# Kernel tuning notes

Measured on AMD Instinct MI355X. Metric: run time of the kernel, lower is better.

Reference implementation:

```python
import jax, jax.numpy as jnp
import numpy as np

N = 50000        # nodes
E = 1600000      # edges (avg degree 32)
DIM_IN = 128
H = 4            # num_heads
D1 = 100         # gc1 per-head out dim
D2 = 20          # gc2 per-head out dim
B = 64           # graphs in the batch
EPS = 1e-5
SLOPE = 0.01     # torch leaky_relu default


def setup_inputs() -> dict:
    key = jax.random.key(0)
    ks = jax.random.split(key, 16)
    sc = lambda fan: 1.0 / np.sqrt(fan)
    inp = {
        'feat': jax.random.normal(ks[0], (N, DIM_IN), jnp.float32),
        'src': jax.random.randint(ks[1], (E,), 0, N, jnp.int32),
        'dst': jax.random.randint(ks[2], (E,), 0, N, jnp.int32),
        'graph_id': jnp.sort(jax.random.randint(ks[3], (N,), 0, B, jnp.int32)),
        # GAT layer 1: per-head fc weight [H, din, dout], attn vector [H, 2*dout]
        'W1': jax.random.normal(ks[4], (H, DIM_IN, D1), jnp.float32) * sc(DIM_IN),
        'a1': jax.random.normal(ks[5], (H, 2 * D1), jnp.float32) * sc(2 * D1),
        # GAT layer 2 (input is cat of heads: H*D1 = 400)
        'W2': jax.random.normal(ks[6], (H, H * D1, D2), jnp.float32) * sc(H * D1),
        'a2': jax.random.normal(ks[7], (H, 2 * D2), jnp.float32) * sc(2 * D2),
        # readout MLP 20 -> 128 -> 32 -> 1
        'Wf1': jax.random.normal(ks[8], (D2, 128), jnp.float32) * sc(D2),
        'bf1': jnp.zeros((128,), jnp.float32),
        'Wf2': jax.random.normal(ks[9], (128, 32), jnp.float32) * sc(128),
        'bf2': jnp.zeros((32,), jnp.float32),
        'Wf3': jax.random.normal(ks[10], (32, 1), jnp.float32) * sc(32),
        'bf3': jnp.zeros((1,), jnp.float32),
        'gamma2': jnp.ones((32,), jnp.float32),   # bn2 weight
        'beta2': jnp.zeros((32,), jnp.float32),   # bn2 bias
    }
    return inp


def _gat_heads(h, W, a, src, dst):
    """Per-head GAT: gather-attn -> segment softmax over dst mailboxes -> scatter-sum.
    Returns list of [N, dout] head outputs. Loop over H=4 heads (small fixed set)."""
    outs = []
    for i in range(W.shape[0]):
        z = h @ W[i]                               # [N, dout]
        d = z.shape[1]
        s_src = z @ a[i, :d]                       # [N] (attn split: a.[z_src,z_dst])
        s_dst = z @ a[i, d:]                       # [N]
        e = jax.nn.leaky_relu(s_src[src] + s_dst[dst], SLOPE)   # [E]
        m = jax.ops.segment_max(e, dst, num_segments=N)          # stable softmax max
        ex = jnp.exp(e - m[dst])
        den = jax.ops.segment_sum(ex, dst, num_segments=N)
        alpha = ex / den[dst]                      # [E] segment softmax
        outs.append(jax.ops.segment_sum(alpha[:, None] * z[src], dst, num_segments=N))
    return outs


def reference(feat, src, dst, graph_id, W1, a1, W2, a2,
              Wf1, bf1, Wf2, bf2, Wf3, bf3, gamma2, beta2):
    src = src.astype(jnp.int32); dst = dst.astype(jnp.int32)
    h = jax.nn.relu(jnp.concatenate(_gat_heads(feat, W1, a1, src, dst), axis=1))  # [N,400]
    h = jax.nn.relu(jnp.mean(jnp.stack(_gat_heads(h, W2, a2, src, dst), 0), 0))   # [N,20]
    # dgl.mean_nodes: per-graph mean of node features
    counts = jax.ops.segment_sum(jnp.ones((N,), h.dtype), graph_id, num_segments=B)
    hg = jax.ops.segment_sum(h, graph_id, num_segments=B) / counts[:, None]        # [B,20]
    out = jax.nn.relu(hg @ Wf1 + bf1)              # dropout = identity (eval)
    out = out @ Wf2 + bf2                          # [B,32]
    mu = jnp.mean(out, axis=0)                     # BatchNorm1d (training stats, biased var)
    var = jnp.mean((out - mu) ** 2, axis=0)
    out = jax.nn.relu(gamma2 * (out - mu) * jax.lax.rsqrt(var + EPS) + beta2)
    return out @ Wf3 + bf3                         # [B,1]
```

## Files before the change

kernel.cpp:

```cpp
#include <hip/hip_runtime.h>
#include <hip/hip_bf16.h>
#include <math.h>

#define N_NODES 50000
#define N_EDGES 1600000
#define DIN 128
#define NH 4
#define D1 100
#define D2 20
#define NB 64
#define EPS_BN 1e-5f


typedef unsigned int uint;
typedef unsigned short ushort;
typedef short short8v __attribute__((ext_vector_type(8)));
typedef float float4v __attribute__((ext_vector_type(4)));

__device__ __forceinline__ void bf16x2_unpack(uint p, float& lo, float& hi) {
  lo = __uint_as_float(p << 16);
  hi = __uint_as_float(p & 0xffff0000u);
}

__device__ __forceinline__ ushort f2bf(float f) {
  uint u = __float_as_uint(f);
  return (ushort)((u + 0x7fffu + ((u >> 16) & 1u)) >> 16);
}

__global__ void prep_b1t(const float* __restrict__ W1, ushort* __restrict__ B1t) {
  int o = blockIdx.x * 256 + threadIdx.x;
  int h = o >> 14;
  int r = o & 16383;
  int j = r >> 7, k = r & 127;
  float v = (j < D1) ? W1[((size_t)h * DIN + k) * D1 + j] : 0.f;
  B1t[o] = f2bf(v);
}

__global__ void prep_b2t(const float* __restrict__ W2, ushort* __restrict__ B2t) {
  int idx = blockIdx.x * 256 + threadIdx.x;
  if (idx >= 80 * 416) return;
  int c = idx / 416, k = idx - c * 416;
  int h = c / D2, j = c - h * D2;
  float v = (k < NH * D1) ? W2[((size_t)h * (NH * D1) + k) * D2 + j] : 0.f;
  B2t[idx] = f2bf(v);
}

__global__ __launch_bounds__(256) void gemm1_mfma(const float* __restrict__ feat,
                                                  const ushort* __restrict__ B1t,
                                                  ushort* __restrict__ z1b) {
  __shared__ __align__(16) short As[64 * 136];
  __shared__ __align__(16) short Bs[128 * 136];
  const int row0 = blockIdx.x * 64;
  const int h = blockIdx.y;
  const int tid = threadIdx.x;
#pragma unroll
  for (int it = 0; it < 8; it++) {
    int idx = tid + it * 256;
    int r = idx >> 5, c4 = idx & 31;
    int row = row0 + r;
    float4 v = make_float4(0.f, 0.f, 0.f, 0.f);
    if (row < N_NODES) v = *reinterpret_cast<const float4*>(feat + (size_t)row * DIN + c4 * 4);
    short4 s;
    s.x = (short)f2bf(v.x); s.y = (short)f2bf(v.y);
    s.z = (short)f2bf(v.z); s.w = (short)f2bf(v.w);
    *reinterpret_cast<short4*>(&As[r * 136 + c4 * 4]) = s;
  }
  {
    const uint* bsrc = reinterpret_cast<const uint*>(B1t + (size_t)h * 16384);
#pragma unroll
    for (int it = 0; it < 32; it++) {
      int idx = tid + it * 256;
      int j = idx >> 6, kk = idx & 63;
      *reinterpret_cast<uint*>(&Bs[j * 136 + kk * 2]) = bsrc[idx];
    }
  }
  __syncthreads();
  const int wv = tid >> 6, lane = tid & 63;
  const int m = lane & 15, q = lane >> 4;
  float4v acc[8];
#pragma unroll
  for (int t = 0; t < 8; t++) acc[t] = (float4v){0.f, 0.f, 0.f, 0.f};
#pragma unroll
  for (int kq = 0; kq < 4; kq++) {
    short8v a = *reinterpret_cast<const short8v*>(&As[(wv * 16 + m) * 136 + kq * 32 + q * 8]);
#pragma unroll
    for (int t = 0; t < 8; t++) {
      short8v b = *reinterpret_cast<const short8v*>(&Bs[(t * 16 + m) * 136 + kq * 32 + q * 8]);
      acc[t] = __builtin_amdgcn_mfma_f32_16x16x32_bf16(a, b, acc[t], 0, 0, 0);
    }
  }
#pragma unroll
  for (int t = 0; t < 8; t++) {
    int cl = t * 16 + m;
    if (cl < D1) {
#pragma unroll
      for (int reg = 0; reg < 4; reg++) {
        int row = row0 + wv * 16 + q * 4 + reg;
        if (row < N_NODES) z1b[(size_t)row * (NH * D1) + h * D1 + cl] = f2bf(acc[t][reg]);
      }
    }
  }
}

__global__ __launch_bounds__(256) void gemm2_mfma(const ushort* __restrict__ h1b,
                                                  const ushort* __restrict__ B2t,
                                                  ushort* __restrict__ z2b) {
  __shared__ __align__(16) short As[64 * 40];
  __shared__ __align__(16) short Bs[80 * 40];
  const int row0 = blockIdx.x * 64;
  const int tid = threadIdx.x;
  const int wv = tid >> 6, lane = tid & 63;
  const int m = lane & 15, q = lane >> 4;
  const uint* au = reinterpret_cast<const uint*>(h1b);
  const uint* bu = reinterpret_cast<const uint*>(B2t);
  uint* asu = reinterpret_cast<uint*>(As);
  uint* bsu = reinterpret_cast<uint*>(Bs);
  float4v acc[5];
#pragma unroll
  for (int t = 0; t < 5; t++) acc[t] = (float4v){0.f, 0.f, 0.f, 0.f};
  for (int ch = 0; ch < 13; ch++) {
    int k0u = ch * 16;
    {
      int idx = tid;
#pragma unroll
      for (int it = 0; it < 4; it++, idx += 256) {
        int r = idx >> 4, ku = idx & 15;
        int row = row0 + r;
        uint v = 0;
        if (row < N_NODES && (k0u + ku) < 200) v = au[(size_t)row * 200 + k0u + ku];
        asu[r * 20 + ku] = v;
      }
      idx = tid;
#pragma unroll
      for (int it = 0; it < 5; it++, idx += 256) {
        int c = idx >> 4, ku = idx & 15;
        bsu[c * 20 + ku] = bu[(size_t)c * 208 + k0u + ku];
      }
    }
    __syncthreads();
    short8v a = *reinterpret_cast<const short8v*>(&As[(wv * 16 + m) * 40 + q * 8]);
#pragma unroll
    for (int t = 0; t < 5; t++) {
      short8v b = *reinterpret_cast<const short8v*>(&Bs[(t * 16 + m) * 40 + q * 8]);
      acc[t] = __builtin_amdgcn_mfma_f32_16x16x32_bf16(a, b, acc[t], 0, 0, 0);
    }
    __syncthreads();
  }
#pragma unroll
  for (int t = 0; t < 5; t++) {
    int col = t * 16 + m;
#pragma unroll
    for (int reg = 0; reg < 4; reg++) {
      int row = row0 + wv * 16 + q * 4 + reg;
      if (row < N_NODES) z2b[(size_t)row * (NH * D2) + col] = f2bf(acc[t][reg]);
    }
  }
}

template <int DOUT>
__global__ void scores_kernel(const ushort* __restrict__ z,
                              const float* __restrict__ a,
                              float* __restrict__ ssrc,
                              float* __restrict__ sdst) {
  int t = blockIdx.x * blockDim.x + threadIdx.x;
  if (t >= N_NODES * NH) return;
  int n = t >> 2;
  int h = t & 3;
  const uint* zr = reinterpret_cast<const uint*>(z) + (size_t)n * (NH * DOUT / 2) + h * (DOUT / 2);
  const float* as = a + h * 2 * DOUT;
  const float* ad = as + DOUT;
  float s1 = 0.f, s2 = 0.f;
  for (int j = 0; j < DOUT / 2; j++) {
    float lo, hi;
    bf16x2_unpack(zr[j], lo, hi);
    s1 += lo * as[2 * j] + hi * as[2 * j + 1];
    s2 += lo * ad[2 * j] + hi * ad[2 * j + 1];
  }
  ssrc[h * N_NODES + n] = s1;
  sdst[h * N_NODES + n] = s2;
}

__global__ void hist_kernel(const int* __restrict__ dst, int* __restrict__ cnt) {
  int e = blockIdx.x * blockDim.x + threadIdx.x;
  if (e < N_EDGES) atomicAdd(&cnt[dst[e]], 1);
}

__global__ __launch_bounds__(512) void scan1_kernel(const int* __restrict__ cnt,
                                                    int* __restrict__ row_ptr,
                                                    int* __restrict__ btot, int n) {
  __shared__ int ws[8];
  int b = blockIdx.x, tid = threadIdx.x, lane = tid & 63, wv = tid >> 6;
  int i = b * 512 + tid;
  int v = (i < n) ? cnt[i] : 0;
  int orig = v;
  for (int off = 1; off < 64; off <<= 1) {
    int t = __shfl_up(v, off);
    if (lane >= off) v += t;
  }
  if (lane == 63) ws[wv] = v;
  __syncthreads();
  int wo = 0;
  for (int j = 0; j < wv; j++) wo += ws[j];
  if (i < n) row_ptr[i] = wo + v - orig;
  if (tid == 511) btot[b] = wo + v;
}

__global__ __launch_bounds__(128) void scan2_kernel(int* __restrict__ btot,
                                                    int* __restrict__ row_ptr_n, int nb) {
  __shared__ int ws2[2];
  int tid = threadIdx.x, lane = tid & 63, wv = tid >> 6;
  int v = (tid < nb) ? btot[tid] : 0;
  int orig = v;
  for (int off = 1; off < 64; off <<= 1) {
    int t = __shfl_up(v, off);
    if (lane >= off) v += t;
  }
  if (lane == 63) ws2[wv] = v;
  __syncthreads();
  int wo = (wv == 1) ? ws2[0] : 0;
  if (tid < nb) btot[tid] = wo + v - orig;
  if (tid == nb - 1) *row_ptr_n = wo + v;
}

__global__ __launch_bounds__(512) void scan3_kernel(int* __restrict__ row_ptr,
                                                    int* __restrict__ cursor,
                                                    const int* __restrict__ btot, int n) {
  int i = blockIdx.x * 512 + threadIdx.x;
  if (i < n) {
    int v = row_ptr[i] + btot[blockIdx.x];
    row_ptr[i] = v;
    cursor[i] = v;
  }
}

__global__ void fill_kernel(const int* __restrict__ src, const int* __restrict__ dst,
                            int* __restrict__ cursor, int* __restrict__ csr_src) {
  int e = blockIdx.x * blockDim.x + threadIdx.x;
  if (e < N_EDGES) {
    int p = atomicAdd(&cursor[dst[e]], 1);
    csr_src[p] = src[e];
  }
}

__global__ __launch_bounds__(256) void agg1_kernel(const ushort* __restrict__ z,
                                                   const float* __restrict__ ssrc,
                                                   const float* __restrict__ sdst,
                                                   const int* __restrict__ row_ptr,
                                                   const int* __restrict__ csr_src,
                                                   ushort* __restrict__ h1b) {
  __shared__ float lw[NH][128];
  const int d = blockIdx.x;
  const int h = threadIdx.x >> 6, lane = threadIdx.x & 63;
  const int beg = row_ptr[d], end = row_ptr[d + 1];
  const int deg = end - beg;
  uint* h1u = reinterpret_cast<uint*>(h1b);
  const size_t ou = (size_t)d * 200 + h * 50 + lane;
  const bool act = lane < D1 / 2;
  if (deg == 0) {
    if (act) h1u[ou] = 0u;
    return;
  }
  const int hN = h * N_NODES;
  const float sd = sdst[hN + d];
  const uint* zb = reinterpret_cast<const uint*>(z);
  const int hco = h * 50 + lane;
  float den = 0.f;
  float aE0 = 0.f, aE1 = 0.f, aE2 = 0.f, aE3 = 0.f;
  float aO0 = 0.f, aO1 = 0.f, aO2 = 0.f, aO3 = 0.f;
  for (int c0 = 0; c0 < deg; c0 += 128) {
    const int cn = min(128, deg - c0);
    const int cb = beg + c0;
    for (int i = lane; i < cn; i += 64) {
      int s = csr_src[cb + i];
      float e = ssrc[hN + s] + sd;
      e = fmaxf(e, 0.01f * e);
      float x = __expf(e);
      lw[h][i] = x;
      den += x;
    }
    if (act) {
      int j = 0;
      for (; j + 8 <= cn; j += 8) {
        int s0 = csr_src[cb + j + 0], s1 = csr_src[cb + j + 1];
        int s2 = csr_src[cb + j + 2], s3 = csr_src[cb + j + 3];
        int s4 = csr_src[cb + j + 4], s5 = csr_src[cb + j + 5];
        int s6 = csr_src[cb + j + 6], s7 = csr_src[cb + j + 7];
        float x0 = lw[h][j + 0], x1 = lw[h][j + 1];
        float x2 = lw[h][j + 2], x3 = lw[h][j + 3];
        float x4 = lw[h][j + 4], x5 = lw[h][j + 5];
        float x6 = lw[h][j + 6], x7 = lw[h][j + 7];
        uint p0 = zb[(size_t)s0 * 200 + hco];
        uint p1 = zb[(size_t)s1 * 200 + hco];
        uint p2 = zb[(size_t)s2 * 200 + hco];
        uint p3 = zb[(size_t)s3 * 200 + hco];
        uint p4 = zb[(size_t)s4 * 200 + hco];
        uint p5 = zb[(size_t)s5 * 200 + hco];
        uint p6 = zb[(size_t)s6 * 200 + hco];
        uint p7 = zb[(size_t)s7 * 200 + hco];
        float lo, hi;
        bf16x2_unpack(p0, lo, hi); aE0 += x0 * lo; aO0 += x0 * hi;
        bf16x2_unpack(p1, lo, hi); aE1 += x1 * lo; aO1 += x1 * hi;
        bf16x2_unpack(p2, lo, hi); aE2 += x2 * lo; aO2 += x2 * hi;
        bf16x2_unpack(p3, lo, hi); aE3 += x3 * lo; aO3 += x3 * hi;
        bf16x2_unpack(p4, lo, hi); aE0 += x4 * lo; aO0 += x4 * hi;
        bf16x2_unpack(p5, lo, hi); aE1 += x5 * lo; aO1 += x5 * hi;
        bf16x2_unpack(p6, lo, hi); aE2 += x6 * lo; aO2 += x6 * hi;
        bf16x2_unpack(p7, lo, hi); aE3 += x7 * lo; aO3 += x7 * hi;
      }
      for (; j < cn; j++) {
        int s = csr_src[cb + j];
        float x = lw[h][j];
        uint p = zb[(size_t)s * 200 + hco];
        float lo, hi;
        bf16x2_unpack(p, lo, hi);
        aE0 += x * lo;
        aO0 += x * hi;
      }
    }
  }
#pragma unroll
  for (int off = 32; off > 0; off >>= 1) den += __shfl_xor(den, off);
  if (!act) return;
  float inv = 1.0f / den;
  float vE = ((aE0 + aE1) + (aE2 + aE3)) * inv;
  float vO = ((aO0 + aO1) + (aO2 + aO3)) * inv;
  vE = vE > 0.f ? vE : 0.f;
  vO = vO > 0.f ? vO : 0.f;
  h1u[ou] = (uint)f2bf(vE) | ((uint)f2bf(vO) << 16);
}

__global__ __launch_bounds__(256) void agg2_kernel(const ushort* __restrict__ z,
                                                   const float* __restrict__ ssrc,
                                                   const float* __restrict__ sdst,
                                                   const int* __restrict__ row_ptr,
                                                   const int* __restrict__ csr_src,
                                                   float* __restrict__ h2) {
  __shared__ float lw[NH][128];
  __shared__ float hbuf[NH][D2];
  const int d = blockIdx.x;
  const int h = threadIdx.x >> 6, lane = threadIdx.x & 63;
  const int beg = row_ptr[d], end = row_ptr[d + 1];
  const int deg = end - beg;
  const int g = lane / 10;
  const int j = lane - g * 10;
  if (deg > 0) {
    const int hN = h * N_NODES;
    const float sd = sdst[hN + d];
    const uint* zb = reinterpret_cast<const uint*>(z);
    const int hco = h * 10 + j;
    float den = 0.f, aE = 0.f, aO = 0.f;
    for (int c0 = 0; c0 < deg; c0 += 128) {
      const int cn = min(128, deg - c0);
      const int cb = beg + c0;
      for (int i = lane; i < cn; i += 64) {
        int s = csr_src[cb + i];
        float e = ssrc[hN + s] + sd;
        e = fmaxf(e, 0.01f * e);
        float x = __expf(e);
        lw[h][i] = x;
        den += x;
      }
      if (g < 6) {
        int i = g;
        for (; i + 6 < cn; i += 12) {
          int s0 = csr_src[cb + i];
          int s1 = csr_src[cb + i + 6];
          float x0 = lw[h][i];
          float x1 = lw[h][i + 6];
          uint p0 = zb[(size_t)s0 * 40 + hco];
          uint p1 = zb[(size_t)s1 * 40 + hco];
          float lo, hi;
          bf16x2_unpack(p0, lo, hi); aE += x0 * lo; aO += x0 * hi;
          bf16x2_unpack(p1, lo, hi); aE += x1 * lo; aO += x1 * hi;
        }
        if (i < cn) {
          int s = csr_src[cb + i];
          float x = lw[h][i];
          uint p = zb[(size_t)s * 40 + hco];
          float lo, hi;
          bf16x2_unpack(p, lo, hi);
          aE += x * lo;
          aO += x * hi;
        }
      }
    }
#pragma unroll
    for (int off = 32; off > 0; off >>= 1) den += __shfl_xor(den, off);
    float tE = aE, tO = aO;
#pragma unroll
    for (int k = 1; k < 6; k++) {
      tE += __shfl(aE, lane + 10 * k);
      tO += __shfl(aO, lane + 10 * k);
    }
    if (lane < 10) {
      float invd = 1.0f / den;
      hbuf[h][2 * j] = tE * invd;
      hbuf[h][2 * j + 1] = tO * invd;
    }
  } else {
    if (lane < 10) {
      hbuf[h][2 * j] = 0.f;
      hbuf[h][2 * j + 1] = 0.f;
    }
  }
  __syncthreads();
  if (threadIdx.x < D2) {
    int c = threadIdx.x;
    float m = 0.25f * (hbuf[0][c] + hbuf[1][c] + hbuf[2][c] + hbuf[3][c]);
    h2[(size_t)d * D2 + c] = m > 0.f ? m : 0.f;
  }
}

__global__ __launch_bounds__(256) void pool_kernel(const float* __restrict__ h2,
                                                   const int* __restrict__ gid,
                                                   float* __restrict__ hg,
                                                   int* __restrict__ gcnt) {
  int wave = threadIdx.x >> 6, lane = threadIdx.x & 63;
  int n = (blockIdx.x * 4 + wave) * 64 + lane;
  bool valid = n < N_NODES;
  int g = gid[valid ? n : (N_NODES - 1)];
  int g0 = __shfl(g, 0), g63 = __shfl(g, 63);
  unsigned long long mask = __ballot(valid);
  if (g0 == g63) {
    if (lane == 0) atomicAdd(&gcnt[g0], (int)__popcll(mask));
#pragma unroll
    for (int c = 0; c < D2; c++) {
      float v = valid ? h2[(size_t)n * D2 + c] : 0.f;
#pragma unroll
      for (int off = 32; off > 0; off >>= 1) v += __shfl_xor(v, off);
      if (lane == 0) atomicAdd(&hg[g0 * D2 + c], v);
    }
  } else if (valid) {
    atomicAdd(&gcnt[g], 1);
    for (int c = 0; c < D2; c++) atomicAdd(&hg[g * D2 + c], h2[(size_t)n * D2 + c]);
  }
}

__global__ __launch_bounds__(256) void head_kernel(const float* __restrict__ hg,
                                                   const int* __restrict__ gcnt,
                                                   const float* __restrict__ Wf1,
                                                   const float* __restrict__ bf1,
                                                   const float* __restrict__ Wf2,
                                                   const float* __restrict__ bf2,
                                                   const float* __restrict__ Wf3,
                                                   const float* __restrict__ bf3,
                                                   const float* __restrict__ gamma,
                                                   const float* __restrict__ beta,
                                                   float* __restrict__ out) {
  __shared__ float X[NB][D2];
  __shared__ float T1[NB][128];
  __shared__ float T2[NB][32];
  __shared__ float scale_s[32], shift_s[32];
  int tid = threadIdx.x;
  for (int i = tid; i < NB * D2; i += 256) {
    int r = i / D2, c = i % D2;
    X[r][c] = hg[i] / (float)gcnt[r];
  }
  __syncthreads();
  for (int i = tid; i < NB * 128; i += 256) {
    int r = i >> 7, c = i & 127;
    float s = bf1[c];
#pragma unroll
    for (int k = 0; k < D2; k++) s += X[r][k] * Wf1[k * 128 + c];
    T1[r][c] = s > 0.f ? s : 0.f;
  }
  __syncthreads();
  for (int i = tid; i < NB * 32; i += 256) {
    int r = i >> 5, c = i & 31;
    float s = bf2[c];
#pragma unroll
    for (int k = 0; k < 128; k++) s += T1[r][k] * Wf2[k * 32 + c];
    T2[r][c] = s;
  }
  __syncthreads();
  if (tid < 32) {
    float mu = 0.f;
    for (int r = 0; r < NB; r++) mu += T2[r][tid];
    mu *= (1.f / NB);
    float var = 0.f;
    for (int r = 0; r < NB; r++) {
      float dv = T2[r][tid] - mu;
      var += dv * dv;
    }
    var *= (1.f / NB);
    float sc = gamma[tid] * rsqrtf(var + EPS_BN);
    scale_s[tid] = sc;
    shift_s[tid] = beta[tid] - mu * sc;
  }
  __syncthreads();
  if (tid < NB) {
    float s = bf3[0];
#pragma unroll
    for (int c = 0; c < 32; c++) {
      float y = scale_s[c] * T2[tid][c] + shift_s[c];
      y = y > 0.f ? y : 0.f;
      s += y * Wf3[c];
    }
    out[tid] = s;
  }
}


extern "C" void kernel_launch(void* const* d_in, const int* in_sizes, int n_in,
                              void* d_out, int out_size, void* d_ws, size_t ws_size,
                              hipStream_t stream) {
  const float* feat = (const float*)d_in[0];
  const int* src = (const int*)d_in[1];
  const int* dst = (const int*)d_in[2];
  const int* gid = (const int*)d_in[3];
  const float* W1 = (const float*)d_in[4];
  const float* a1 = (const float*)d_in[5];
  const float* W2 = (const float*)d_in[6];
  const float* a2 = (const float*)d_in[7];
  const float* Wf1 = (const float*)d_in[8];
  const float* bf1 = (const float*)d_in[9];
  const float* Wf2 = (const float*)d_in[10];
  const float* bf2 = (const float*)d_in[11];
  const float* Wf3 = (const float*)d_in[12];
  const float* bf3 = (const float*)d_in[13];
  const float* gamma2 = (const float*)d_in[14];
  const float* beta2 = (const float*)d_in[15];
  float* outp = (float*)d_out;

  char* p = (char*)d_ws;
  auto alloc = [&](size_t bytes) {
    void* q = (void*)p;
    p += (bytes + 255) & ~(size_t)255;
    return q;
  };
  ushort* z1b = (ushort*)alloc((size_t)N_NODES * NH * D1 * 2);
  ushort* z2b = (ushort*)alloc((size_t)N_NODES * NH * D2 * 2);
  ushort* h1b = (ushort*)alloc((size_t)N_NODES * NH * D1 * 2);
  float* h2 = (float*)alloc((size_t)N_NODES * D2 * 4);
  float* ssrc = (float*)alloc((size_t)NH * N_NODES * 4);
  float* sdst = (float*)alloc((size_t)NH * N_NODES * 4);
  int* cnt = (int*)alloc((size_t)N_NODES * 4);
  int* row_ptr = (int*)alloc((size_t)(N_NODES + 1) * 4);
  int* cursor = (int*)alloc((size_t)N_NODES * 4);
  int* csr = (int*)alloc((size_t)N_EDGES * 4);
  int* btot = (int*)alloc((size_t)128 * 4);
  ushort* B1t = (ushort*)alloc((size_t)NH * 128 * 128 * 2);
  ushort* B2t = (ushort*)alloc((size_t)80 * 416 * 2);
  float* hg = (float*)alloc((size_t)NB * D2 * 4);
  int* gcnt = (int*)alloc((size_t)NB * 4);

  const int rows64 = (N_NODES + 63) / 64;
  const int eblk = (N_EDGES + 255) / 256;
  const int nblk = (N_NODES + 255) / 256;
  const int nhblk = (N_NODES * NH + 255) / 256;
  const int sblk = (N_NODES + 511) / 512;

  hipMemsetAsync(cnt, 0, (size_t)N_NODES * 4, stream);
  hist_kernel<<<eblk, 256, 0, stream>>>(dst, cnt);
  scan1_kernel<<<sblk, 512, 0, stream>>>(cnt, row_ptr, btot, N_NODES);
  scan2_kernel<<<1, 128, 0, stream>>>(btot, row_ptr + N_NODES, sblk);
  scan3_kernel<<<sblk, 512, 0, stream>>>(row_ptr, cursor, btot, N_NODES);
  fill_kernel<<<eblk, 256, 0, stream>>>(src, dst, cursor, csr);

  prep_b1t<<<256, 256, 0, stream>>>(W1, B1t);
  prep_b2t<<<130, 256, 0, stream>>>(W2, B2t);

  gemm1_mfma<<<dim3(rows64, NH), 256, 0, stream>>>(feat, B1t, z1b);
  scores_kernel<D1><<<nhblk, 256, 0, stream>>>(z1b, a1, ssrc, sdst);
  agg1_kernel<<<N_NODES, 256, 0, stream>>>(z1b, ssrc, sdst, row_ptr, csr, h1b);

  gemm2_mfma<<<rows64, 256, 0, stream>>>(h1b, B2t, z2b);
  scores_kernel<D2><<<nhblk, 256, 0, stream>>>(z2b, a2, ssrc, sdst);
  agg2_kernel<<<N_NODES, 256, 0, stream>>>(z2b, ssrc, sdst, row_ptr, csr, h2);

  hipMemsetAsync(hg, 0, (size_t)NB * D2 * 4, stream);
  hipMemsetAsync(gcnt, 0, (size_t)NB * 4, stream);
  pool_kernel<<<nblk, 256, 0, stream>>>(h2, gid, hg, gcnt);
  head_kernel<<<1, 256, 0, stream>>>(hg, gcnt, Wf1, bf1, Wf2, bf2, Wf3, bf3,
                                     gamma2, beta2, outp);
}
```

Baseline: 760.5 us.

## Pad z layouts per head and gather edges with 16-byte vector loads

The projected node features z1 and z2 are stored with per-head padding (104 and 24 bf16 elements per head), so each head slice is 16-byte aligned. The aggregation kernels then gather neighbour rows with uint4 loads. Lanes are split into groups that each handle different edges, and partial sums are combined with cross-lane shuffles. This cuts the number of gather instructions per edge and improves memory-transaction efficiency. In exchange it adds padding bytes, shuffle reductions, and partly idle lanes (for example, 13 of 16 lanes active per group in agg1).

Measured after the change: 797.8 us. 1.05x slower.

```diff
diff --git a/kernel.cpp b/kernel.cpp
--- a/kernel.cpp
+++ b/kernel.cpp
@@ -16,6 +16,12 @@
 typedef unsigned short ushort;
 typedef short short8v __attribute__((ext_vector_type(8)));
 typedef float float4v __attribute__((ext_vector_type(4)));
+typedef uint uint4v __attribute__((ext_vector_type(4)));
+
+#define Z1_ROWU 208
+#define Z1_HU 52
+#define Z2_ROWU 48
+#define Z2_HU 12
 
 __device__ __forceinline__ void bf16x2_unpack(uint p, float& lo, float& hi) {
   lo = __uint_as_float(p << 16);
@@ -92,11 +98,12 @@
 #pragma unroll
   for (int t = 0; t < 8; t++) {
     int cl = t * 16 + m;
-    if (cl < D1) {
+    if (cl < 104) {
 #pragma unroll
       for (int reg = 0; reg < 4; reg++) {
         int row = row0 + wv * 16 + q * 4 + reg;
-        if (row < N_NODES) z1b[(size_t)row * (NH * D1) + h * D1 + cl] = f2bf(acc[t][reg]);
+        if (row < N_NODES)
+          z1b[(size_t)row * 416 + h * 104 + cl] = (cl < D1) ? f2bf(acc[t][reg]) : (ushort)0;
       }
     }
   }
@@ -149,15 +156,17 @@
 #pragma unroll
   for (int t = 0; t < 5; t++) {
     int col = t * 16 + m;
+    int hh = col / 20;
+    int jj = col - hh * 20;
 #pragma unroll
     for (int reg = 0; reg < 4; reg++) {
       int row = row0 + wv * 16 + q * 4 + reg;
-      if (row < N_NODES) z2b[(size_t)row * (NH * D2) + col] = f2bf(acc[t][reg]);
-    }
-  }
-}
-
-template <int DOUT>
+      if (row < N_NODES) z2b[(size_t)row * 96 + hh * 24 + jj] = f2bf(acc[t][reg]);
+    }
+  }
+}
+
+template <int DOUT, int HEADU, int ROWU>
 __global__ void scores_kernel(const ushort* __restrict__ z,
                               const float* __restrict__ a,
                               float* __restrict__ ssrc,
@@ -166,7 +175,7 @@
   if (t >= N_NODES * NH) return;
   int n = t >> 2;
   int h = t & 3;
-  const uint* zr = reinterpret_cast<const uint*>(z) + (size_t)n * (NH * DOUT / 2) + h * (DOUT / 2);
+  const uint* zr = reinterpret_cast<const uint*>(z) + (size_t)n * ROWU + h * HEADU;
   const float* as = a + h * 2 * DOUT;
   const float* ad = as + DOUT;
   float s1 = 0.f, s2 = 0.f;
@@ -251,22 +260,28 @@
   __shared__ float lw[NH][128];
   const int d = blockIdx.x;
   const int h = threadIdx.x >> 6, lane = threadIdx.x & 63;
+  const int g = lane >> 4;
+  const int j = lane & 15;
   const int beg = row_ptr[d], end = row_ptr[d + 1];
   const int deg = end - beg;
   uint* h1u = reinterpret_cast<uint*>(h1b);
-  const size_t ou = (size_t)d * 200 + h * 50 + lane;
-  const bool act = lane < D1 / 2;
   if (deg == 0) {
-    if (act) h1u[ou] = 0u;
+    if (g == 0 && j < 13) {
+      int base = d * 200 + h * 50 + j * 4;
+      int nu = (j == 12) ? 2 : 4;
+      for (int u = 0; u < nu; u++) h1u[base + u] = 0u;
+    }
     return;
   }
   const int hN = h * N_NODES;
   const float sd = sdst[hN + d];
-  const uint* zb = reinterpret_cast<const uint*>(z);
-  const int hco = h * 50 + lane;
+  const uint* zu = reinterpret_cast<const uint*>(z);
+  const int zoff = h * Z1_HU + j * 4;
+  const bool act = (j < 13);
   float den = 0.f;
-  float aE0 = 0.f, aE1 = 0.f, aE2 = 0.f, aE3 = 0.f;
-  float aO0 = 0.f, aO1 = 0.f, aO2 = 0.f, aO3 = 0.f;
+  float acc[8];
+#pragma unroll
+  for (int t = 0; t < 8; t++) acc[t] = 0.f;
   for (int c0 = 0; c0 < deg; c0 += 128) {
     const int cn = min(128, deg - c0);
     const int cb = beg + c0;
@@ -279,54 +294,39 @@
       den += x;
     }
     if (act) {
-      int j = 0;
-      for (; j + 8 <= cn; j += 8) {
-        int s0 = csr_src[cb + j + 0], s1 = csr_src[cb + j + 1];
-        int s2 = csr_src[cb + j + 2], s3 = csr_src[cb + j + 3];
-        int s4 = csr_src[cb + j + 4], s5 = csr_src[cb + j + 5];
-        int s6 = csr_src[cb + j + 6], s7 = csr_src[cb + j + 7];
-        float x0 = lw[h][j + 0], x1 = lw[h][j + 1];
-        float x2 = lw[h][j + 2], x3 = lw[h][j + 3];
-        float x4 = lw[h][j + 4], x5 = lw[h][j + 5];
-        float x6 = lw[h][j + 6], x7 = lw[h][j + 7];
-        uint p0 = zb[(size_t)s0 * 200 + hco];
-        uint p1 = zb[(size_t)s1 * 200 + hco];
-        uint p2 = zb[(size_t)s2 * 200 + hco];
-        uint p3 = zb[(size_t)s3 * 200 + hco];
-        uint p4 = zb[(size_t)s4 * 200 + hco];
-        uint p5 = zb[(size_t)s5 * 200 + hco];
-        uint p6 = zb[(size_t)s6 * 200 + hco];
-        uint p7 = zb[(size_t)s7 * 200 + hco];
+      for (int i = g; i < cn; i += 4) {
+        int s = csr_src[cb + i];
+        float x = lw[h][i];
+        uint4v p = *reinterpret_cast<const uint4v*>(zu + (size_t)s * Z1_ROWU + zoff);
         float lo, hi;
-        bf16x2_unpack(p0, lo, hi); aE0 += x0 * lo; aO0 += x0 * hi;
-        bf16x2_unpack(p1, lo, hi); aE1 += x1 * lo; aO1 += x1 * hi;
-        bf16x2_unpack(p2, lo, hi); aE2 += x2 * lo; aO2 += x2 * hi;
-        bf16x2_unpack(p3, lo, hi); aE3 += x3 * lo; aO3 += x3 * hi;
-        bf16x2_unpack(p4, lo, hi); aE0 += x4 * lo; aO0 += x4 * hi;
-        bf16x2_unpack(p5, lo, hi); aE1 += x5 * lo; aO1 += x5 * hi;
-        bf16x2_unpack(p6, lo, hi); aE2 += x6 * lo; aO2 += x6 * hi;
-        bf16x2_unpack(p7, lo, hi); aE3 += x7 * lo; aO3 += x7 * hi;
-      }
-      for (; j < cn; j++) {
-        int s = csr_src[cb + j];
-        float x = lw[h][j];
-        uint p = zb[(size_t)s * 200 + hco];
-        float lo, hi;
-        bf16x2_unpack(p, lo, hi);
-        aE0 += x * lo;
-        aO0 += x * hi;
+        bf16x2_unpack(p.x, lo, hi); acc[0] += x * lo; acc[1] += x * hi;
+        bf16x2_unpack(p.y, lo, hi); acc[2] += x * lo; acc[3] += x * hi;
+        bf16x2_unpack(p.z, lo, hi); acc[4] += x * lo; acc[5] += x * hi;
+        bf16x2_unpack(p.w, lo, hi); acc[6] += x * lo; acc[7] += x * hi;
       }
     }
   }
 #pragma unroll
   for (int off = 32; off > 0; off >>= 1) den += __shfl_xor(den, off);
-  if (!act) return;
+#pragma unroll
+  for (int t = 0; t < 8; t++) {
+    acc[t] += __shfl_xor(acc[t], 32);
+    acc[t] += __shfl_xor(acc[t], 16);
+  }
+  if (g != 0 || j >= 13) return;
   float inv = 1.0f / den;
-  float vE = ((aE0 + aE1) + (aE2 + aE3)) * inv;
-  float vO = ((aO0 + aO1) + (aO2 + aO3)) * inv;
-  vE = vE > 0.f ? vE : 0.f;
-  vO = vO > 0.f ? vO : 0.f;
-  h1u[ou] = (uint)f2bf(vE) | ((uint)f2bf(vO) << 16);
+  int base = d * 200 + h * 50 + j * 4;
+  int nu = (j == 12) ? 2 : 4;
+#pragma unroll
+  for (int u = 0; u < 4; u++) {
+    if (u < nu) {
+      float vE = acc[2 * u] * inv;
+      float vO = acc[2 * u + 1] * inv;
+      vE = vE > 0.f ? vE : 0.f;
+      vO = vO > 0.f ? vO : 0.f;
+      h1u[base + u] = (uint)f2bf(vE) | ((uint)f2bf(vO) << 16);
+    }
+  }
 }
 
 __global__ __launch_bounds__(256) void agg2_kernel(const ushort* __restrict__ z,
@@ -339,16 +339,20 @@
   __shared__ float hbuf[NH][D2];
   const int d = blockIdx.x;
   const int h = threadIdx.x >> 6, lane = threadIdx.x & 63;
+  const int g = lane >> 2;
+  const int j = lane & 3;
   const int beg = row_ptr[d], end = row_ptr[d + 1];
   const int deg = end - beg;
-  const int g = lane / 10;
-  const int j = lane - g * 10;
   if (deg > 0) {
     const int hN = h * N_NODES;
     const float sd = sdst[hN + d];
-    const uint* zb = reinterpret_cast<const uint*>(z);
-    const int hco = h * 10 + j;
-    float den = 0.f, aE = 0.f, aO = 0.f;
+    const uint* zu = reinterpret_cast<const uint*>(z);
+    const int zoff = h * Z2_HU + j * 4;
+    const bool act = (j < 3);
+    float den = 0.f;
+    float acc[8];
+#pragma unroll
+    for (int t = 0; t < 8; t++) acc[t] = 0.f;
     for (int c0 = 0; c0 < deg; c0 += 128) {
       const int cn = min(128, deg - c0);
       const int cb = beg + c0;
@@ -360,47 +364,43 @@
         lw[h][i] = x;
         den += x;
       }
-      if (g < 6) {
-        int i = g;
-        for (; i + 6 < cn; i += 12) {
-          int s0 = csr_src[cb + i];
-          int s1 = csr_src[cb + i + 6];
-          float x0 = lw[h][i];
-          float x1 = lw[h][i + 6];
-          uint p0 = zb[(size_t)s0 * 40 + hco];
-          uint p1 = zb[(size_t)s1 * 40 + hco];
-          float lo, hi;
-          bf16x2_unpack(p0, lo, hi); aE += x0 * lo; aO += x0 * hi;
-          bf16x2_unpack(p1, lo, hi); aE += x1 * lo; aO += x1 * hi;
-        }
-        if (i < cn) {
+      if (act) {
+        for (int i = g; i < cn; i += 16) {
           int s = csr_src[cb + i];
           float x = lw[h][i];
-          uint p = zb[(size_t)s * 40 + hco];
+          uint4v p = *reinterpret_cast<const uint4v*>(zu + (size_t)s * Z2_ROWU + zoff);
           float lo, hi;
-          bf16x2_unpack(p, lo, hi);
-          aE += x * lo;
-          aO += x * hi;
+          bf16x2_unpack(p.x, lo, hi); acc[0] += x * lo; acc[1] += x * hi;
+          bf16x2_unpack(p.y, lo, hi); acc[2] += x * lo; acc[3] += x * hi;
+          bf16x2_unpack(p.z, lo, hi); acc[4] += x * lo; acc[5] += x * hi;
+          bf16x2_unpack(p.w, lo, hi); acc[6] += x * lo; acc[7] += x * hi;
         }
       }
     }
 #pragma unroll
     for (int off = 32; off > 0; off >>= 1) den += __shfl_xor(den, off);
-    float tE = aE, tO = aO;
-#pragma unroll
-    for (int k = 1; k < 6; k++) {
-      tE += __shfl(aE, lane + 10 * k);
-      tO += __shfl(aO, lane + 10 * k);
-    }
-    if (lane < 10) {
+#pragma unroll
+    for (int t = 0; t < 8; t++) {
+      acc[t] += __shfl_xor(acc[t], 4);
+      acc[t] += __shfl_xor(acc[t], 8);
+      acc[t] += __shfl_xor(acc[t], 16);
+      acc[t] += __shfl_xor(acc[t], 32);
+    }
+    if (lane < 3) {
       float invd = 1.0f / den;
-      hbuf[h][2 * j] = tE * invd;
-      hbuf[h][2 * j + 1] = tO * invd;
+#pragma unroll
+      for (int t = 0; t < 8; t++) {
+        int c = lane * 8 + t;
+        if (c < D2) hbuf[h][c] = acc[t] * invd;
+      }
     }
   } else {
-    if (lane < 10) {
-      hbuf[h][2 * j] = 0.f;
-      hbuf[h][2 * j + 1] = 0.f;
+    if (lane < 3) {
+#pragma unroll
+      for (int t = 0; t < 8; t++) {
+        int c = lane * 8 + t;
+        if (c < D2) hbuf[h][c] = 0.f;
+      }
     }
   }
   __syncthreads();
@@ -528,8 +528,8 @@
     p += (bytes + 255) & ~(size_t)255;
     return q;
   };
-  ushort* z1b = (ushort*)alloc((size_t)N_NODES * NH * D1 * 2);
-  ushort* z2b = (ushort*)alloc((size_t)N_NODES * NH * D2 * 2);
+  ushort* z1b = (ushort*)alloc((size_t)N_NODES * 416 * 2);
+  ushort* z2b = (ushort*)alloc((size_t)N_NODES * 96 * 2);
   ushort* h1b = (ushort*)alloc((size_t)N_NODES * NH * D1 * 2);
   float* h2 = (float*)alloc((size_t)N_NODES * D2 * 4);
   float* ssrc = (float*)alloc((size_t)NH * N_NODES * 4);
@@ -561,11 +561,11 @@
   prep_b2t<<<130, 256, 0, stream>>>(W2, B2t);
 
   gemm1_mfma<<<dim3(rows64, NH), 256, 0, stream>>>(feat, B1t, z1b);
-  scores_kernel<D1><<<nhblk, 256, 0, stream>>>(z1b, a1, ssrc, sdst);
+  scores_kernel<D1, Z1_HU, Z1_ROWU><<<nhblk, 256, 0, stream>>>(z1b, a1, ssrc, sdst);
   agg1_kernel<<<N_NODES, 256, 0, stream>>>(z1b, ssrc, sdst, row_ptr, csr, h1b);
 
   gemm2_mfma<<<rows64, 256, 0, stream>>>(h1b, B2t, z2b);
-  scores_kernel<D2><<<nhblk, 256, 0, stream>>>(z2b, a2, ssrc, sdst);
+  scores_kernel<D2, Z2_HU, Z2_ROWU><<<nhblk, 256, 0, stream>>>(z2b, a2, ssrc, sdst);
   agg2_kernel<<<N_NODES, 256, 0, stream>>>(z2b, ssrc, sdst, row_ptr, csr, h2);
 
   hipMemsetAsync(hg, 0, (size_t)NB * D2 * 4, stream);
```

## Pad z1/z2 rows to aligned strides and restructure agg2 to split edges across waves

Applied to the files above, without the earlier changes.

The z1 buffer is stored with a padded 448-element row (104 per head) and z2 with a 128-element row, so each gathered neighbour row begins on a larger aligned boundary and the agg kernels' row gathers touch fewer cache lines. agg2 is rewritten so each of the 4 waves handles a strided slice of 8-edge chunks covering all heads at once. It uses 40 lanes to gather an 80-element z2 row per edge, then reduces the partial sums and denominators across waves in shared memory. This raises parallelism per destination node and coalesces gathers, at the cost of more memory for the padded buffers and some idle lanes.

New measurement: 733.0 us. 1.04x faster.

```diff
diff --git a/kernel.cpp b/kernel.cpp
--- a/kernel.cpp
+++ b/kernel.cpp
@@ -16,6 +16,10 @@
 typedef unsigned short ushort;
 typedef short short8v __attribute__((ext_vector_type(8)));
 typedef float float4v __attribute__((ext_vector_type(4)));
+
+#define Z1_ROWU 224
+#define Z1_HU 52
+#define Z2_ROWU 64
 
 __device__ __forceinline__ void bf16x2_unpack(uint p, float& lo, float& hi) {
   lo = __uint_as_float(p << 16);
@@ -92,11 +96,12 @@
 #pragma unroll
   for (int t = 0; t < 8; t++) {
     int cl = t * 16 + m;
-    if (cl < D1) {
+    if (cl < 104) {
 #pragma unroll
       for (int reg = 0; reg < 4; reg++) {
         int row = row0 + wv * 16 + q * 4 + reg;
-        if (row < N_NODES) z1b[(size_t)row * (NH * D1) + h * D1 + cl] = f2bf(acc[t][reg]);
+        if (row < N_NODES)
+          z1b[(size_t)row * 448 + h * 104 + cl] = (cl < D1) ? f2bf(acc[t][reg]) : (ushort)0;
       }
     }
   }
@@ -152,12 +157,12 @@
 #pragma unroll
     for (int reg = 0; reg < 4; reg++) {
       int row = row0 + wv * 16 + q * 4 + reg;
-      if (row < N_NODES) z2b[(size_t)row * (NH * D2) + col] = f2bf(acc[t][reg]);
-    }
-  }
-}
-
-template <int DOUT>
+      if (row < N_NODES) z2b[(size_t)row * 128 + col] = f2bf(acc[t][reg]);
+    }
+  }
+}
+
+template <int DOUT, int HEADU, int ROWU>
 __global__ void scores_kernel(const ushort* __restrict__ z,
                               const float* __restrict__ a,
                               float* __restrict__ ssrc,
@@ -166,7 +171,7 @@
   if (t >= N_NODES * NH) return;
   int n = t >> 2;
   int h = t & 3;
-  const uint* zr = reinterpret_cast<const uint*>(z) + (size_t)n * (NH * DOUT / 2) + h * (DOUT / 2);
+  const uint* zr = reinterpret_cast<const uint*>(z) + (size_t)n * ROWU + h * HEADU;
   const float* as = a + h * 2 * DOUT;
   const float* ad = as + DOUT;
   float s1 = 0.f, s2 = 0.f;
@@ -263,7 +268,7 @@
   const int hN = h * N_NODES;
   const float sd = sdst[hN + d];
   const uint* zb = reinterpret_cast<const uint*>(z);
-  const int hco = h * 50 + lane;
+  const int hco = h * Z1_HU + lane;
   float den = 0.f;
   float aE0 = 0.f, aE1 = 0.f, aE2 = 0.f, aE3 = 0.f;
   float aO0 = 0.f, aO1 = 0.f, aO2 = 0.f, aO3 = 0.f;
@@ -289,14 +294,14 @@
         float x2 = lw[h][j + 2], x3 = lw[h][j + 3];
         float x4 = lw[h][j + 4], x5 = lw[h][j + 5];
         float x6 = lw[h][j + 6], x7 = lw[h][j + 7];
-        uint p0 = zb[(size_t)s0 * 200 + hco];
-        uint p1 = zb[(size_t)s1 * 200 + hco];
-        uint p2 = zb[(size_t)s2 * 200 + hco];
-        uint p3 = zb[(size_t)s3 * 200 + hco];
-        uint p4 = zb[(size_t)s4 * 200 + hco];
-        uint p5 = zb[(size_t)s5 * 200 + hco];
-        uint p6 = zb[(size_t)s6 * 200 + hco];
-        uint p7 = zb[(size_t)s7 * 200 + hco];
+        uint p0 = zb[(size_t)s0 * Z1_ROWU + hco];
+        uint p1 = zb[(size_t)s1 * Z1_ROWU + hco];
+        uint p2 = zb[(size_t)s2 * Z1_ROWU + hco];
+        uint p3 = zb[(size_t)s3 * Z1_ROWU + hco];
+        uint p4 = zb[(size_t)s4 * Z1_ROWU + hco];
+        uint p5 = zb[(size_t)s5 * Z1_ROWU + hco];
+        uint p6 = zb[(size_t)s6 * Z1_ROWU + hco];
+        uint p7 = zb[(size_t)s7 * Z1_ROWU + hco];
         float lo, hi;
         bf16x2_unpack(p0, lo, hi); aE0 += x0 * lo; aO0 += x0 * hi;
         bf16x2_unpack(p1, lo, hi); aE1 += x1 * lo; aO1 += x1 * hi;
@@ -310,7 +315,7 @@
       for (; j < cn; j++) {
         int s = csr_src[cb + j];
         float x = lw[h][j];
-        uint p = zb[(size_t)s * 200 + hco];
+        uint p = zb[(size_t)s * Z1_ROWU + hco];
         float lo, hi;
         bf16x2_unpack(p, lo, hi);
         aE0 += x * lo;
@@ -335,79 +340,77 @@
                                                    const int* __restrict__ row_ptr,
                                                    const int* __restrict__ csr_src,
                                                    float* __restrict__ h2) {
-  __shared__ float lw[NH][128];
-  __shared__ float hbuf[NH][D2];
+  __shared__ float xw[4][8][4];
+  __shared__ int sw[4][8];
+  __shared__ float accb[4][40][2];
+  __shared__ float denb[4][4];
   const int d = blockIdx.x;
-  const int h = threadIdx.x >> 6, lane = threadIdx.x & 63;
-  const int beg = row_ptr[d], end = row_ptr[d + 1];
-  const int deg = end - beg;
-  const int g = lane / 10;
-  const int j = lane - g * 10;
-  if (deg > 0) {
-    const int hN = h * N_NODES;
-    const float sd = sdst[hN + d];
-    const uint* zb = reinterpret_cast<const uint*>(z);
-    const int hco = h * 10 + j;
-    float den = 0.f, aE = 0.f, aO = 0.f;
-    for (int c0 = 0; c0 < deg; c0 += 128) {
-      const int cn = min(128, deg - c0);
-      const int cb = beg + c0;
-      for (int i = lane; i < cn; i += 64) {
-        int s = csr_src[cb + i];
-        float e = ssrc[hN + s] + sd;
-        e = fmaxf(e, 0.01f * e);
-        float x = __expf(e);
-        lw[h][i] = x;
-        den += x;
+  const int wv = threadIdx.x >> 6, lane = threadIdx.x & 63;
+  const int beg = row_ptr[d];
+  const int deg = row_ptr[d + 1] - beg;
+  if (deg == 0) {
+    if (threadIdx.x < D2) h2[(size_t)d * D2 + threadIdx.x] = 0.f;
+    return;
+  }
+  const int eh_h = lane & 3, eh_e = lane >> 2;
+  const int hq = lane / 10;
+  const uint* zu = reinterpret_cast<const uint*>(z);
+  float sd = 0.f;
+  if (lane < 32) sd = sdst[eh_h * N_NODES + d];
+  float den = 0.f;
+  float acc0 = 0.f, acc1 = 0.f;
+  for (int c0 = wv * 8; c0 < deg; c0 += 32) {
+    const int cn = min(8, deg - c0);
+    const int cb = beg + c0;
+    if (lane < 32) {
+      int ee = (eh_e < cn) ? eh_e : 0;
+      int s = csr_src[cb + ee];
+      float e = ssrc[eh_h * N_NODES + s] + sd;
+      e = fmaxf(e, 0.01f * e);
+      float x = (eh_e < cn) ? __expf(e) : 0.f;
+      den += x;
+      xw[wv][eh_e][eh_h] = x;
+      if (eh_h == 0) sw[wv][eh_e] = s;
+    }
+    if (lane < 40) {
+#pragma unroll
+      for (int e = 0; e < 8; e++) {
+        int se = sw[wv][e];
+        float xx = xw[wv][e][hq];
+        uint p = zu[(size_t)se * Z2_ROWU + lane];
+        float lo, hi;
+        bf16x2_unpack(p, lo, hi);
+        acc0 += xx * lo;
+        acc1 += xx * hi;
       }
-      if (g < 6) {
-        int i = g;
-        for (; i + 6 < cn; i += 12) {
-          int s0 = csr_src[cb + i];
-          int s1 = csr_src[cb + i + 6];
-          float x0 = lw[h][i];
-          float x1 = lw[h][i + 6];
-          uint p0 = zb[(size_t)s0 * 40 + hco];
-          uint p1 = zb[(size_t)s1 * 40 + hco];
-          float lo, hi;
-          bf16x2_unpack(p0, lo, hi); aE += x0 * lo; aO += x0 * hi;
-          bf16x2_unpack(p1, lo, hi); aE += x1 * lo; aO += x1 * hi;
-        }
-        if (i < cn) {
-          int s = csr_src[cb + i];
-          float x = lw[h][i];
-          uint p = zb[(size_t)s * 40 + hco];
-          float lo, hi;
-          bf16x2_unpack(p, lo, hi);
-          aE += x * lo;
-          aO += x * hi;
-        }
-      }
-    }
-#pragma unroll
-    for (int off = 32; off > 0; off >>= 1) den += __shfl_xor(den, off);
-    float tE = aE, tO = aO;
-#pragma unroll
-    for (int k = 1; k < 6; k++) {
-      tE += __shfl(aE, lane + 10 * k);
-      tO += __shfl(aO, lane + 10 * k);
-    }
-    if (lane < 10) {
-      float invd = 1.0f / den;
-      hbuf[h][2 * j] = tE * invd;
-      hbuf[h][2 * j + 1] = tO * invd;
-    }
-  } else {
-    if (lane < 10) {
-      hbuf[h][2 * j] = 0.f;
-      hbuf[h][2 * j + 1] = 0.f;
-    }
-  }
-  __syncthreads();
-  if (threadIdx.x < D2) {
-    int c = threadIdx.x;
-    float m = 0.25f * (hbuf[0][c] + hbuf[1][c] + hbuf[2][c] + hbuf[3][c]);
-    h2[(size_t)d * D2 + c] = m > 0.f ? m : 0.f;
+    }
+  }
+  den += __shfl_xor(den, 4);
+  den += __shfl_xor(den, 8);
+  den += __shfl_xor(den, 16);
+  if (lane < 4) denb[wv][lane] = den;
+  if (lane < 40) {
+    accb[wv][lane][0] = acc0;
+    accb[wv][lane][1] = acc1;
+  }
+  __syncthreads();
+  if (threadIdx.x < 10) {
+    int j = threadIdx.x;
+    float vE = 0.f, vO = 0.f;
+#pragma unroll
+    for (int h = 0; h < 4; h++) {
+      float dn = denb[0][h] + denb[1][h] + denb[2][h] + denb[3][h];
+      float invd = 1.0f / dn;
+      int sl = h * 10 + j;
+      float lo = accb[0][sl][0] + accb[1][sl][0] + accb[2][sl][0] + accb[3][sl][0];
+      float hi = accb[0][sl][1] + accb[1][sl][1] + accb[2][sl][1] + accb[3][sl][1];
+      vE += lo * invd;
+      vO += hi * invd;
+    }
+    vE *= 0.25f;
+    vO *= 0.25f;
+    h2[(size_t)d * D2 + 2 * j] = vE > 0.f ? vE : 0.f;
+    h2[(size_t)d * D2 + 2 * j + 1] = vO > 0.f ? vO : 0.f;
   }
 }
 
@@ -528,8 +531,8 @@
     p += (bytes + 255) & ~(size_t)255;
     return q;
   };
-  ushort* z1b = (ushort*)alloc((size_t)N_NODES * NH * D1 * 2);
-  ushort* z2b = (ushort*)alloc((size_t)N_NODES * NH * D2 * 2);
+  ushort* z1b = (ushort*)alloc((size_t)N_NODES * 448 * 2);
+  ushort* z2b = (ushort*)alloc((size_t)N_NODES * 128 * 2);
   ushort* h1b = (ushort*)alloc((size_t)N_NODES * NH * D1 * 2);
   float* h2 = (float*)alloc((size_t)N_NODES * D2 * 4);
   float* ssrc = (float*)alloc((size_t)NH * N_NODES * 4);
@@ -561,11 +564,11 @@
   prep_b2t<<<130, 256, 0, stream>>>(W2, B2t);
 
   gemm1_mfma<<<dim3(rows64, NH), 256, 0, stream>>>(feat, B1t, z1b);
-  scores_kernel<D1><<<nhblk, 256, 0, stream>>>(z1b, a1, ssrc, sdst);
+  scores_kernel<D1, Z1_HU, Z1_ROWU><<<nhblk, 256, 0, stream>>>(z1b, a1, ssrc, sdst);
   agg1_kernel<<<N_NODES, 256, 0, stream>>>(z1b, ssrc, sdst, row_ptr, csr, h1b);
 
   gemm2_mfma<<<rows64, 256, 0, stream>>>(h1b, B2t, z2b);
-  scores_kernel<D2><<<nhblk, 256, 0, stream>>>(z2b, a2, ssrc, sdst);
+  scores_kernel<D2, 10, Z2_ROWU><<<nhblk, 256, 0, stream>>>(z2b, a2, ssrc, sdst);
   agg2_kernel<<<N_NODES, 256, 0, stream>>>(z2b, ssrc, sdst, row_ptr, csr, h2);
 
   hipMemsetAsync(hg, 0, (size_t)NB * D2 * 4, stream);
```
